# Performance work log

Measured on AMD Instinct MI355X. Metric: run time of the kernel, lower is better.

Reference implementation:

```python
import jax, jax.numpy as jnp
import numpy as np

N = 100000   # nodes
E = 600000   # edges
G = 4096     # graphs in batch
D_IN = 73
D_E = 101
D = 128      # latent_dim
BN_EPS = 1e-5


def _bn(h, gamma, beta):
    # BatchNorm1d in training mode: batch statistics (biased variance)
    m = h.mean(axis=0)
    v = h.var(axis=0)
    return (h - m) * jax.lax.rsqrt(v + BN_EPS) * gamma + beta


def setup_inputs() -> dict:
    key = jax.random.key(0)
    ks = jax.random.split(key, 24)
    inp = {
        "x": jax.random.normal(ks[0], (N, D_IN), jnp.float32),
        "edge_attr": jax.random.normal(ks[1], (E, D_E), jnp.float32),
        "src": jax.random.randint(ks[2], (E,), 0, N, jnp.int32),
        "dst": jax.random.randint(ks[3], (E,), 0, N, jnp.int32),
        "batch": jnp.sort(jax.random.randint(ks[4], (N,), 0, G, jnp.int32)),
        # node embedding Linear(73 -> 128)
        "W_emb": jax.random.normal(ks[5], (D_IN, D), jnp.float32) / np.sqrt(D_IN),
        "b_emb": jnp.zeros((D,), jnp.float32),
    }
    k = 6
    for i in range(2):
        inp[f"We{i}"] = jax.random.normal(ks[k], (D_E, D), jnp.float32) / np.sqrt(D_E); k += 1
        inp[f"be{i}"] = jnp.zeros((D,), jnp.float32)
        inp[f"W1_{i}"] = jax.random.normal(ks[k], (D, 2 * D), jnp.float32) / np.sqrt(D); k += 1
        inp[f"b1_{i}"] = jnp.zeros((2 * D,), jnp.float32)
        inp[f"g1_{i}"] = jnp.ones((2 * D,), jnp.float32)
        inp[f"bb1_{i}"] = jnp.zeros((2 * D,), jnp.float32)
        inp[f"W2_{i}"] = jax.random.normal(ks[k], (2 * D, D), jnp.float32) / np.sqrt(2 * D); k += 1
        inp[f"b2_{i}"] = jnp.zeros((D,), jnp.float32)
        inp[f"go_{i}"] = jnp.ones((D,), jnp.float32)
        inp[f"bo_{i}"] = jnp.zeros((D,), jnp.float32)
    return inp


def _forward(x, edge_attr, src, dst, batch,
             W_emb, b_emb,
             We0, be0, W1_0, b1_0, g1_0, bb1_0, W2_0, b2_0, go_0, bo_0,
             We1, be1, W1_1, b1_1, g1_1, bb1_1, W2_1, b2_1, go_1, bo_1):
    layers = [
        (We0, be0, W1_0, b1_0, g1_0, bb1_0, W2_0, b2_0, go_0, bo_0),
        (We1, be1, W1_1, b1_1, g1_1, bb1_1, W2_1, b2_1, go_1, bo_1),
    ]
    h = x @ W_emb + b_emb  # [N, D]
    n_layers = len(layers)
    for i, (We, be, W1, b1, g1, bb1, W2, b2, go, bo) in enumerate(layers):
        e = edge_attr @ We + be                         # [E, D]
        msg = jax.nn.relu(h[src] + e)                   # gather + add + ReLU
        agg = jax.ops.segment_sum(msg, dst, num_segments=N)  # scatter-sum
        z = h + agg                                     # (1 + eps) * x_i + aggr, eps = 0
        z = jax.nn.relu(_bn(z @ W1 + b1, g1, bb1))      # MLP: Linear -> BN -> ReLU
        h = _bn(z @ W2 + b2, go, bo)                    # Linear -> outer BN
        if i != n_layers - 1:
            h = jax.nn.relu(h)
        # dropout p=0 -> identity
    # global mean pool over graphs
    sums = jax.ops.segment_sum(h, batch, num_segments=G)            # [G, D]
    counts = jax.ops.segment_sum(jnp.ones((h.shape[0],), h.dtype), batch, num_segments=G)
    return sums / jnp.maximum(counts, 1.0)[:, None]


def reference(x, edge_attr, src, dst, batch,
              W_emb, b_emb,
              We0, be0, W1_0, b1_0, g1_0, bb1_0, W2_0, b2_0, go_0, bo_0,
              We1, be1, W1_1, b1_1, g1_1, bb1_1, W2_1, b2_1, go_1, bo_1):
    return _forward(x, edge_attr, src, dst, batch, W_emb, b_emb,
                    We0, be0, W1_0, b1_0, g1_0, bb1_0, W2_0, b2_0, go_0, bo_0,
                    We1, be1, W1_1, b1_1, g1_1, bb1_1, W2_1, b2_1, go_1, bo_1)
```

## Files before the change

kernel.cpp:

```cpp
#include <hip/hip_runtime.h>
#include <cstddef>

#define NN  100000
#define NE  600000
#define NG  4096
#define DIN 73
#define DE  101
#define DD  128
#define DD2 256
#define NP  100096
#define EP  600064

typedef unsigned int uint;
typedef unsigned short ushort;
typedef __attribute__((ext_vector_type(8))) short bf16x8;
typedef __attribute__((ext_vector_type(4))) float f32x4;

__device__ __forceinline__ void fadd_atomic(float* p, float v) { unsafeAtomicAdd(p, v); }

__device__ __forceinline__ ushort f2bf(float f) {
    uint u = __float_as_uint(f);
    uint r = (u + 0x7fffu + ((u >> 16) & 1u)) >> 16;
    return (ushort)r;
}
__device__ __forceinline__ float bf2f(ushort u) { return __uint_as_float(((uint)u) << 16); }

__device__ __forceinline__ bf16x8 ld_zfrag(const float* __restrict__ p) {
    const float4 f0 = *(const float4*)p;
    const float4 f1 = *(const float4*)(p + 4);
    bf16x8 r;
    r[0] = (short)f2bf(f0.x); r[1] = (short)f2bf(f0.y);
    r[2] = (short)f2bf(f0.z); r[3] = (short)f2bf(f0.w);
    r[4] = (short)f2bf(f1.x); r[5] = (short)f2bf(f1.y);
    r[6] = (short)f2bf(f1.z); r[7] = (short)f2bf(f1.w);
    return r;
}


__global__ void hist_kernel(const int* __restrict__ dst, int* __restrict__ deg) {
    int e = blockIdx.x * blockDim.x + threadIdx.x;
    if (e < NE) atomicAdd(&deg[dst[e]], 1);
}

__global__ __launch_bounds__(256) void scan_chunk_kernel(
    const int* __restrict__ deg, int* __restrict__ offs, int* __restrict__ csums)
{
    const int b = blockIdx.x, t = threadIdx.x;
    const int base = b * 1024 + t * 4;
    int v[4];
    #pragma unroll
    for (int i = 0; i < 4; ++i) v[i] = (base + i < NN) ? deg[base + i] : 0;
    int tsum = v[0] + v[1] + v[2] + v[3];
    const int lane = t & 63, w = t >> 6;
    int x = tsum;
    #pragma unroll
    for (int d = 1; d < 64; d <<= 1) {
        int y = __shfl_up(x, d, 64);
        if (lane >= d) x += y;
    }
    __shared__ int wsum[4];
    if (lane == 63) wsum[w] = x;
    __syncthreads();
    int woff = 0;
    for (int i = 0; i < w; ++i) woff += wsum[i];
    int run = woff + x - tsum;
    #pragma unroll
    for (int i = 0; i < 4; ++i) {
        if (base + i < NN) offs[base + i] = run;
        run += v[i];
    }
    if (t == 255) csums[b] = woff + x;
}

__global__ void scan_tops_kernel(int* __restrict__ csums, int* __restrict__ offs, int nchunks) {
    if (threadIdx.x == 0 && blockIdx.x == 0) {
        int run = 0;
        for (int i = 0; i < nchunks; ++i) { int c = csums[i]; csums[i] = run; run += c; }
        offs[NN] = run;
    }
}

__global__ void scan_add_kernel(int* __restrict__ offs, const int* __restrict__ csums) {
    int i = blockIdx.x * blockDim.x + threadIdx.x;
    if (i < NN) offs[i] += csums[i >> 10];
}

__global__ void scatter_kernel(const int* __restrict__ dst, const int* __restrict__ src,
                               const int* __restrict__ offs, int* __restrict__ cursor,
                               int* __restrict__ eperm, int* __restrict__ srcp,
                               int* __restrict__ dstp)
{
    int e = blockIdx.x * blockDim.x + threadIdx.x;
    if (e >= NE) return;
    int d = dst[e];
    int pos = offs[d] + atomicAdd(&cursor[d], 1);
    eperm[e] = pos;
    srcp[pos] = src[e];
    dstp[pos] = d;
}

__global__ void gstart_kernel(const int* __restrict__ batch, int* __restrict__ gstart) {
    int n = blockIdx.x * blockDim.x + threadIdx.x;
    if (n > NN) return;
    if (n == NN) {
        for (int g = batch[NN - 1] + 1; g <= NG; ++g) gstart[g] = NN;
        return;
    }
    int b = batch[n];
    int pb = (n == 0) ? -1 : batch[n - 1];
    for (int g = pb + 1; g <= b; ++g) gstart[g] = n;
}


__global__ __launch_bounds__(256) void cvt_ea_kernel(const float* __restrict__ ea,
                                                     const int* __restrict__ eperm,
                                                     ushort* __restrict__ eabc)
{
    const int t = threadIdx.x;
    const int r = blockIdx.x * 8 + (t >> 5);
    if (r >= NE) return;
    const int pos = eperm[r];
    const int c = (t & 31) * 4;
    ushort4 o;
    #pragma unroll
    for (int i = 0; i < 4; ++i) {
        const int col = c + i;
        float v = (col < DE) ? ea[(size_t)r * DE + col] : ((col == DE) ? 1.0f : 0.0f);
        ((ushort*)&o)[i] = f2bf(v);
    }
    *(ushort4*)&eabc[(size_t)pos * 128 + c] = o;
}

__global__ void cvt_wt_kernel(const float* __restrict__ in, ushort* __restrict__ out,
                              int Kin, int Nn, int Kp, const float* __restrict__ bias)
{
    const int n = blockIdx.x;
    for (int k = threadIdx.x; k < Kp; k += blockDim.x) {
        float v = 0.0f;
        if (k < Kin) v = in[(size_t)k * Nn + n];
        else if (k == Kin && bias) v = bias[n];
        out[(size_t)n * Kp + k] = f2bf(v);
    }
}

__global__ __launch_bounds__(256, 2) void edge_agg_kernel(
    const ushort* __restrict__ eab, const ushort* __restrict__ Wt,
    const int* __restrict__ srcp, const int* __restrict__ dstp,
    const ushort* __restrict__ hb, float* __restrict__ zf)
{
    __shared__ ushort vals[128 * 128];
    __shared__ int nd[128];
    const int tid = threadIdx.x;
    const int wid = tid >> 6;
    const int msub = wid >> 1, nsl = wid & 1;
    const int lane = tid & 63, l15 = lane & 15, grp = lane >> 4;
    const int n0 = nsl * 64;

    bf16x8 A[4][4];
    #pragma unroll
    for (int nf = 0; nf < 4; ++nf)
        #pragma unroll
        for (int kk = 0; kk < 4; ++kk)
            A[nf][kk] = *(const bf16x8*)(Wt + (size_t)(n0 + nf * 16 + l15) * 128 + kk * 32 + grp * 8);

    const int rcol = tid & 127;
    const int rh   = tid >> 7;

    const int ntiles = EP / 128;
    for (int t = blockIdx.x; t < ntiles; t += gridDim.x) {
        const int r0 = t * 128;
        const int m0 = r0 + msub * 64;
        __syncthreads();
        if (tid < 128) {
            const int rr = r0 + tid;
            nd[tid] = (rr < NE) ? dstp[rr] : NN;
        }
        int sp[4];
        #pragma unroll
        for (int mf = 0; mf < 4; ++mf) {
            const int rr = m0 + mf * 16 + l15;
            sp[mf] = (rr < NE) ? srcp[rr] : 0;
        }
        ushort4 hv[4][4];
        #pragma unroll
        for (int mf = 0; mf < 4; ++mf)
            #pragma unroll
            for (int nf = 0; nf < 4; ++nf)
                hv[mf][nf] = *(const ushort4*)&hb[(size_t)sp[mf] * 128 + n0 + nf * 16 + grp * 4];
        f32x4 acc[4][4];
        #pragma unroll
        for (int i = 0; i < 4; ++i)
            #pragma unroll
            for (int j = 0; j < 4; ++j) acc[i][j] = (f32x4){0.f, 0.f, 0.f, 0.f};
        #pragma unroll
        for (int kk = 0; kk < 4; ++kk) {
            bf16x8 b[4];
            #pragma unroll
            for (int mf = 0; mf < 4; ++mf)
                b[mf] = *(const bf16x8*)(eab + (size_t)(m0 + mf * 16 + l15) * 128 + kk * 32 + grp * 8);
            #pragma unroll
            for (int mf = 0; mf < 4; ++mf)
                #pragma unroll
                for (int nf = 0; nf < 4; ++nf)
                    acc[mf][nf] = __builtin_amdgcn_mfma_f32_16x16x32_bf16(A[nf][kk], b[mf], acc[mf][nf], 0, 0, 0);
        }
        #pragma unroll
        for (int mf = 0; mf < 4; ++mf) {
            const int row = msub * 64 + mf * 16 + l15;
            const int sw = (row & 7) << 3;
            #pragma unroll
            for (int nf = 0; nf < 4; ++nf) {
                const int col = n0 + nf * 16 + grp * 4;
                ushort4 o;
                o.x = f2bf(fmaxf(acc[mf][nf][0] + bf2f(hv[mf][nf].x), 0.f));
                o.y = f2bf(fmaxf(acc[mf][nf][1] + bf2f(hv[mf][nf].y), 0.f));
                o.z = f2bf(fmaxf(acc[mf][nf][2] + bf2f(hv[mf][nf].z), 0.f));
                o.w = f2bf(fmaxf(acc[mf][nf][3] + bf2f(hv[mf][nf].w), 0.f));
                *(ushort4*)&vals[row * 128 + (col ^ sw)] = o;
            }
        }
        __syncthreads();
        float accs = 0.f;
        int cur = nd[rh * 64];
        for (int r = rh * 64; r < rh * 64 + 64; ++r) {
            const int node = nd[r];
            const float v = bf2f(vals[r * 128 + (rcol ^ ((r & 7) << 3))]);
            if (node != cur) {
                if (cur < NN) fadd_atomic(&zf[(size_t)cur * 128 + rcol], accs);
                accs = 0.f; cur = node;
            }
            accs += v;
        }
        if (cur < NN) fadd_atomic(&zf[(size_t)cur * 128 + rcol], accs);
    }
}

__global__ void zinit_kernel(const ushort* __restrict__ hb, float* __restrict__ zf) {
    int i = blockIdx.x * blockDim.x + threadIdx.x;
    const int stride = gridDim.x * blockDim.x;
    for (; i < NP * 32; i += stride) {
        const int n = i >> 5;
        float4 o;
        if (n < NN) {
            ushort4 u = *(const ushort4*)&hb[(size_t)i * 4];
            o.x = bf2f(u.x); o.y = bf2f(u.y); o.z = bf2f(u.z); o.w = bf2f(u.w);
        } else {
            o.x = 0.f; o.y = 0.f; o.z = 0.f; o.w = 0.f;
        }
        *(float4*)&zf[(size_t)i * 4] = o;
    }
}


__global__ __launch_bounds__(256, 2) void mlp1_gemm_kernel(
    const float* __restrict__ z, const ushort* __restrict__ Wt,
    const float* __restrict__ bias, ushort* __restrict__ y)
{
    const int n0 = (threadIdx.x >> 6) * 64;
    const int lane = threadIdx.x & 63, l15 = lane & 15, grp = lane >> 4;
    bf16x8 A[4][4];
    #pragma unroll
    for (int nf = 0; nf < 4; ++nf)
        #pragma unroll
        for (int kk = 0; kk < 4; ++kk)
            A[nf][kk] = *(const bf16x8*)(Wt + (size_t)(n0 + nf * 16 + l15) * 128 + kk * 32 + grp * 8);
    float4 bv[4];
    #pragma unroll
    for (int nf = 0; nf < 4; ++nf) bv[nf] = *(const float4*)&bias[n0 + nf * 16 + grp * 4];

    const int ntiles = NP / 64;
    for (int t = blockIdx.x; t < ntiles; t += gridDim.x) {
        const int m0 = t * 64;
        f32x4 acc[4][4];
        #pragma unroll
        for (int i = 0; i < 4; ++i)
            #pragma unroll
            for (int j = 0; j < 4; ++j) acc[i][j] = (f32x4){0.f, 0.f, 0.f, 0.f};
        #pragma unroll
        for (int kk = 0; kk < 4; ++kk) {
            bf16x8 b[4];
            #pragma unroll
            for (int mf = 0; mf < 4; ++mf)
                b[mf] = ld_zfrag(z + (size_t)(m0 + mf * 16 + l15) * 128 + kk * 32 + grp * 8);
            #pragma unroll
            for (int mf = 0; mf < 4; ++mf)
                #pragma unroll
                for (int nf = 0; nf < 4; ++nf)
                    acc[mf][nf] = __builtin_amdgcn_mfma_f32_16x16x32_bf16(A[nf][kk], b[mf], acc[mf][nf], 0, 0, 0);
        }
        #pragma unroll
        for (int mf = 0; mf < 4; ++mf) {
            ushort* rp = &y[(size_t)(m0 + mf * 16 + l15) * 256 + n0];
            #pragma unroll
            for (int nf = 0; nf < 4; ++nf) {
                ushort4 o;
                o.x = f2bf(acc[mf][nf][0] + bv[nf].x);
                o.y = f2bf(acc[mf][nf][1] + bv[nf].y);
                o.z = f2bf(acc[mf][nf][2] + bv[nf].z);
                o.w = f2bf(acc[mf][nf][3] + bv[nf].w);
                *(ushort4*)&rp[nf * 16 + grp * 4] = o;
            }
        }
    }
}

__global__ __launch_bounds__(256, 2) void mlp2_gemm_kernel(
    const ushort* __restrict__ y1, const ushort* __restrict__ Wt,
    const float* __restrict__ bias, ushort* __restrict__ y2)
{
    const int wid = threadIdx.x >> 6;
    const int msub = wid >> 1, nsl = wid & 1;
    const int lane = threadIdx.x & 63, l15 = lane & 15, grp = lane >> 4;
    const int n0 = nsl * 64;
    bf16x8 A[4][8];
    #pragma unroll
    for (int nf = 0; nf < 4; ++nf)
        #pragma unroll
        for (int kk = 0; kk < 8; ++kk)
            A[nf][kk] = *(const bf16x8*)(Wt + (size_t)(n0 + nf * 16 + l15) * 256 + kk * 32 + grp * 8);
    float4 bv[4];
    #pragma unroll
    for (int nf = 0; nf < 4; ++nf) bv[nf] = *(const float4*)&bias[n0 + nf * 16 + grp * 4];

    const int ntiles = NP / 128;
    for (int t = blockIdx.x; t < ntiles; t += gridDim.x) {
        const int m0 = t * 128 + msub * 64;
        f32x4 acc[4][4];
        #pragma unroll
        for (int i = 0; i < 4; ++i)
            #pragma unroll
            for (int j = 0; j < 4; ++j) acc[i][j] = (f32x4){0.f, 0.f, 0.f, 0.f};
        #pragma unroll
        for (int kk = 0; kk < 8; ++kk) {
            bf16x8 b[4];
            #pragma unroll
            for (int mf = 0; mf < 4; ++mf)
                b[mf] = *(const bf16x8*)(y1 + (size_t)(m0 + mf * 16 + l15) * 256 + kk * 32 + grp * 8);
            #pragma unroll
            for (int mf = 0; mf < 4; ++mf)
                #pragma unroll
                for (int nf = 0; nf < 4; ++nf)
                    acc[mf][nf] = __builtin_amdgcn_mfma_f32_16x16x32_bf16(A[nf][kk], b[mf], acc[mf][nf], 0, 0, 0);
        }
        #pragma unroll
        for (int mf = 0; mf < 4; ++mf) {
            ushort* rp = &y2[(size_t)(m0 + mf * 16 + l15) * 128 + n0];
            #pragma unroll
            for (int nf = 0; nf < 4; ++nf) {
                ushort4 o;
                o.x = f2bf(acc[mf][nf][0] + bv[nf].x);
                o.y = f2bf(acc[mf][nf][1] + bv[nf].y);
                o.z = f2bf(acc[mf][nf][2] + bv[nf].z);
                o.w = f2bf(acc[mf][nf][3] + bv[nf].w);
                *(ushort4*)&rp[nf * 16 + grp * 4] = o;
            }
        }
    }
}


__global__ __launch_bounds__(128) void embed_kernel(
    const float* __restrict__ x, const float* __restrict__ W,
    const float* __restrict__ b, ushort* __restrict__ hb)
{
    __shared__ float xs[4][DIN];
    const int n0 = blockIdx.x * 4;
    const int d  = threadIdx.x;
    for (int idx = d; idx < 4 * DIN; idx += 128) {
        int r = idx / DIN, c = idx - r * DIN;
        xs[r][c] = x[(size_t)n0 * DIN + idx];
    }
    __syncthreads();
    float bb = b[d];
    float a0 = bb, a1 = bb, a2 = bb, a3 = bb;
    for (int k = 0; k < DIN; ++k) {
        float w = W[k * DD + d];
        a0 = fmaf(xs[0][k], w, a0);
        a1 = fmaf(xs[1][k], w, a1);
        a2 = fmaf(xs[2][k], w, a2);
        a3 = fmaf(xs[3][k], w, a3);
    }
    hb[(size_t)(n0 + 0) * DD + d] = f2bf(a0);
    hb[(size_t)(n0 + 1) * DD + d] = f2bf(a1);
    hb[(size_t)(n0 + 2) * DD + d] = f2bf(a2);
    hb[(size_t)(n0 + 3) * DD + d] = f2bf(a3);
}

__global__ __launch_bounds__(256) void colstats256_kernel(
    const ushort* __restrict__ y, float* __restrict__ s, float* __restrict__ q)
{
    const int t = threadIdx.x;
    const int cs = (t & 63) * 4, rg = t >> 6;
    const int r0 = blockIdx.x * 256;
    float ps0 = 0, ps1 = 0, ps2 = 0, ps3 = 0, pq0 = 0, pq1 = 0, pq2 = 0, pq3 = 0;
    for (int i = rg; i < 256; i += 4) {
        const int r = r0 + i;
        if (r >= NN) break;
        ushort4 u = *(const ushort4*)&y[(size_t)r * 256 + cs];
        float f0 = bf2f(u.x), f1 = bf2f(u.y), f2v = bf2f(u.z), f3 = bf2f(u.w);
        ps0 += f0; pq0 += f0 * f0;
        ps1 += f1; pq1 += f1 * f1;
        ps2 += f2v; pq2 += f2v * f2v;
        ps3 += f3; pq3 += f3 * f3;
    }
    __shared__ float SS[4][256], SQ[4][256];
    SS[rg][cs + 0] = ps0; SS[rg][cs + 1] = ps1; SS[rg][cs + 2] = ps2; SS[rg][cs + 3] = ps3;
    SQ[rg][cs + 0] = pq0; SQ[rg][cs + 1] = pq1; SQ[rg][cs + 2] = pq2; SQ[rg][cs + 3] = pq3;
    __syncthreads();
    if (rg == 0) {
        #pragma unroll
        for (int j = 0; j < 4; ++j) {
            const int c = cs + j;
            fadd_atomic(&s[c], SS[0][c] + SS[1][c] + SS[2][c] + SS[3][c]);
            fadd_atomic(&q[c], SQ[0][c] + SQ[1][c] + SQ[2][c] + SQ[3][c]);
        }
    }
}

__global__ __launch_bounds__(256) void colstats128b_kernel(
    const ushort* __restrict__ y, float* __restrict__ s, float* __restrict__ q)
{
    const int t = threadIdx.x;
    const int cs = (t & 31) * 4, rg = t >> 5;
    const int r0 = blockIdx.x * 256;
    float ps0 = 0, ps1 = 0, ps2 = 0, ps3 = 0, pq0 = 0, pq1 = 0, pq2 = 0, pq3 = 0;
    for (int i = rg; i < 256; i += 8) {
        const int r = r0 + i;
        if (r >= NN) break;
        ushort4 u = *(const ushort4*)&y[(size_t)r * 128 + cs];
        float f0 = bf2f(u.x), f1 = bf2f(u.y), f2v = bf2f(u.z), f3 = bf2f(u.w);
        ps0 += f0; pq0 += f0 * f0;
        ps1 += f1; pq1 += f1 * f1;
        ps2 += f2v; pq2 += f2v * f2v;
        ps3 += f3; pq3 += f3 * f3;
    }
    __shared__ float SS[8][128], SQ[8][128];
    SS[rg][cs + 0] = ps0; SS[rg][cs + 1] = ps1; SS[rg][cs + 2] = ps2; SS[rg][cs + 3] = ps3;
    SQ[rg][cs + 0] = pq0; SQ[rg][cs + 1] = pq1; SQ[rg][cs + 2] = pq2; SQ[rg][cs + 3] = pq3;
    __syncthreads();
    if (rg == 0) {
        #pragma unroll
        for (int j = 0; j < 4; ++j) {
            const int c = cs + j;
            float sv = 0, qv = 0;
            #pragma unroll
            for (int g = 0; g < 8; ++g) { sv += SS[g][c]; qv += SQ[g][c]; }
            fadd_atomic(&s[c], sv);
            fadd_atomic(&q[c], qv);
        }
    }
}

__global__ void finalize_kernel(const float* __restrict__ s, const float* __restrict__ sq,
                                const float* __restrict__ g, const float* __restrict__ bb,
                                float* __restrict__ a, float* __restrict__ c,
                                int dim, float invN)
{
    int d = blockIdx.x * blockDim.x + threadIdx.x;
    if (d >= dim) return;
    float m  = s[d] * invN;
    float v  = sq[d] * invN - m * m;
    float rs = rsqrtf(v + 1e-5f);
    float ai = g[d] * rs;
    a[d] = ai;
    c[d] = bb[d] - m * ai;
}

__global__ void bnrelu_bf_kernel(ushort* __restrict__ y, const float* __restrict__ a,
                                 const float* __restrict__ c)
{
    int i = blockIdx.x * blockDim.x + threadIdx.x;
    const int stride = gridDim.x * blockDim.x;
    for (; i < NN * 64; i += stride) {
        const int cb = (i & 63) * 4;
        ushort4 u = *(const ushort4*)&y[(size_t)i * 4];
        const float4 av = *(const float4*)&a[cb];
        const float4 cv = *(const float4*)&c[cb];
        ushort4 o;
        o.x = f2bf(fmaxf(fmaf(bf2f(u.x), av.x, cv.x), 0.f));
        o.y = f2bf(fmaxf(fmaf(bf2f(u.y), av.y, cv.y), 0.f));
        o.z = f2bf(fmaxf(fmaf(bf2f(u.z), av.z, cv.z), 0.f));
        o.w = f2bf(fmaxf(fmaf(bf2f(u.w), av.w, cv.w), 0.f));
        *(ushort4*)&y[(size_t)i * 4] = o;
    }
}

__global__ void bnrelu_hb_kernel(ushort* __restrict__ hb, const float* __restrict__ a,
                                 const float* __restrict__ c)
{
    int i = blockIdx.x * blockDim.x + threadIdx.x;
    const int stride = gridDim.x * blockDim.x;
    for (; i < NN * 32; i += stride) {
        const int cb = (i & 31) * 4;
        ushort4 u = *(const ushort4*)&hb[(size_t)i * 4];
        const float4 av = *(const float4*)&a[cb];
        const float4 cv = *(const float4*)&c[cb];
        ushort4 o;
        o.x = f2bf(fmaxf(fmaf(bf2f(u.x), av.x, cv.x), 0.f));
        o.y = f2bf(fmaxf(fmaf(bf2f(u.y), av.y, cv.y), 0.f));
        o.z = f2bf(fmaxf(fmaf(bf2f(u.z), av.z, cv.z), 0.f));
        o.w = f2bf(fmaxf(fmaf(bf2f(u.w), av.w, cv.w), 0.f));
        *(ushort4*)&hb[(size_t)i * 4] = o;
    }
}

__global__ __launch_bounds__(256) void pool_kernel(
    const ushort* __restrict__ hb, const float* __restrict__ a2, const float* __restrict__ c2,
    const int* __restrict__ gstart, float* __restrict__ out)
{
    const int g = blockIdx.x * 4 + (threadIdx.x >> 6);
    if (g >= NG) return;
    const int lane = threadIdx.x & 63;
    const int s = gstart[g], t = gstart[g + 1];
    float a0 = 0.f, a1 = 0.f;
    for (int n = s; n < t; ++n) {
        const uint v = *(const uint*)&hb[(size_t)n * 128 + lane * 2];
        a0 += __uint_as_float(v << 16);
        a1 += __uint_as_float(v & 0xffff0000u);
    }
    const int d0 = lane * 2;
    float2 o;
    if (t > s) {
        const float inv = 1.0f / (float)(t - s);
        o.x = fmaf(a2[d0 + 0], a0 * inv, c2[d0 + 0]);
        o.y = fmaf(a2[d0 + 1], a1 * inv, c2[d0 + 1]);
    } else {
        o.x = 0.f; o.y = 0.f;
    }
    *(float2*)&out[(size_t)g * 128 + d0] = o;
}


extern "C" void kernel_launch(void* const* d_in, const int* in_sizes, int n_in,
                              void* d_out, int out_size, void* d_ws, size_t ws_size,
                              hipStream_t stream)
{
    (void)in_sizes; (void)n_in; (void)out_size; (void)ws_size;
    const float* x     = (const float*)d_in[0];
    const float* ea    = (const float*)d_in[1];
    const int*   src   = (const int*)d_in[2];
    const int*   dst   = (const int*)d_in[3];
    const int*   batch = (const int*)d_in[4];
    const float* W_emb = (const float*)d_in[5];
    const float* b_emb = (const float*)d_in[6];

    char* ws = (char*)d_ws;
    auto alloc = [&](size_t bytes) { void* p = ws; ws += (bytes + 255) & ~(size_t)255; return p; };

    ushort* hb   = (ushort*)alloc((size_t)NP * 128 * 2);
    float*  zf   = (float*) alloc((size_t)NP * 128 * 4);
    ushort* eabc = (ushort*)alloc((size_t)EP * 128 * 2);
    ushort* y1b  = (ushort*)alloc((size_t)NP * 256 * 2);
    int* deg    = (int*)alloc((size_t)NN * 4);
    int* offs   = (int*)alloc((size_t)(NN + 1) * 4);
    int* eperm  = (int*)alloc((size_t)NE * 4);
    int* srcp   = (int*)alloc((size_t)NE * 4);
    int* dstp   = (int*)alloc((size_t)NE * 4);
    int* csums  = (int*)alloc(128 * 4);
    int* gstart = (int*)alloc((size_t)(NG + 1) * 4);
    ushort* Wet[2], *W1t[2], *W2t[2];
    for (int l = 0; l < 2; ++l) {
        Wet[l] = (ushort*)alloc(128 * 128 * 2);
        W1t[l] = (ushort*)alloc(256 * 128 * 2);
        W2t[l] = (ushort*)alloc(128 * 256 * 2);
    }
    float* st = (float*)alloc(2048 * 4);
    float* s1 = st,        *sq1 = st + 256, *a1 = st + 512,  *c1 = st + 768;
    float* s2 = st + 1024, *sq2 = st + 1152, *a2 = st + 1280, *c2 = st + 1408;
    float* out = (float*)d_out;

    const int NCHUNK = (NN + 1023) / 1024;

    hipMemsetAsync(deg, 0, (size_t)NN * 4, stream);
    hist_kernel<<<(NE + 255) / 256, 256, 0, stream>>>(dst, deg);
    scan_chunk_kernel<<<NCHUNK, 256, 0, stream>>>(deg, offs, csums);
    scan_tops_kernel<<<1, 1, 0, stream>>>(csums, offs, NCHUNK);
    scan_add_kernel<<<(NN + 255) / 256, 256, 0, stream>>>(offs, csums);
    hipMemsetAsync(deg, 0, (size_t)NN * 4, stream);
    scatter_kernel<<<(NE + 255) / 256, 256, 0, stream>>>(dst, src, offs, deg, eperm, srcp, dstp);
    gstart_kernel<<<(NN + 256) / 256, 256, 0, stream>>>(batch, gstart);

    cvt_ea_kernel<<<(NE + 7) / 8, 256, 0, stream>>>(ea, eperm, eabc);
    for (int l = 0; l < 2; ++l) {
        const float* const* L = (const float* const*)(d_in + 7 + l * 10);
        cvt_wt_kernel<<<128, 128, 0, stream>>>(L[0], Wet[l], 101, 128, 128, L[1]);
        cvt_wt_kernel<<<256, 128, 0, stream>>>(L[2], W1t[l], 128, 256, 128, nullptr);
        cvt_wt_kernel<<<128, 128, 0, stream>>>(L[6], W2t[l], 256, 128, 256, nullptr);
    }

    embed_kernel<<<NN / 4, 128, 0, stream>>>(x, W_emb, b_emb, hb);

    for (int layer = 0; layer < 2; ++layer) {
        const float* const* L = (const float* const*)(d_in + 7 + layer * 10);
        const float* b1  = L[3];
        const float* g1  = L[4]; const float* bb1 = L[5];
        const float* b2  = L[7];
        const float* go  = L[8]; const float* bo  = L[9];

        zinit_kernel<<<2048, 256, 0, stream>>>(hb, zf);
        edge_agg_kernel<<<1172, 256, 0, stream>>>(eabc, Wet[layer], srcp, dstp, hb, zf);

        hipMemsetAsync(s1, 0, 512 * sizeof(float), stream);
        hipMemsetAsync(s2, 0, 256 * sizeof(float), stream);

        mlp1_gemm_kernel<<<782, 256, 0, stream>>>(zf, W1t[layer], b1, y1b);
        colstats256_kernel<<<NP / 256 + 1, 256, 0, stream>>>(y1b, s1, sq1);
        finalize_kernel<<<1, 256, 0, stream>>>(s1, sq1, g1, bb1, a1, c1, 256, 1.0f / NN);
        bnrelu_bf_kernel<<<2048, 256, 0, stream>>>(y1b, a1, c1);
        mlp2_gemm_kernel<<<391, 256, 0, stream>>>(y1b, W2t[layer], b2, hb);
        colstats128b_kernel<<<NP / 256 + 1, 256, 0, stream>>>(hb, s2, sq2);
        finalize_kernel<<<1, 128, 0, stream>>>(s2, sq2, go, bo, a2, c2, 128, 1.0f / NN);

        if (layer == 0) {
            bnrelu_hb_kernel<<<2048, 256, 0, stream>>>(hb, a2, c2);
        } else {
            pool_kernel<<<NG / 4, 256, 0, stream>>>(hb, a2, c2, gstart, out);
        }
    }
}
```

Before: 1.039 ms.

## Fuse z initialization into embed and BN-ReLU kernels; unroll edge segmented reduce

Removes the separate zinit kernel, which read hb and wrote the fp32 z buffer. Embed and the layer-0 BN-ReLU kernel now write the fp32 copy directly, saving one full read of hb and one launch per layer. The edge aggregation kernel is tuned as well: occupancy hint raised to 3 blocks per SM, __syncthreads replaced with an explicit lgkmcnt wait plus s_barrier, and the per-column segmented reduction unrolled to batch 8 LDS reads ahead of the atomic logic. The padding rows of zf are no longer zeroed each layer, so correctness depends on that region staying zero from allocation.

```diff
diff --git a/kernel.cpp b/kernel.cpp
--- a/kernel.cpp
+++ b/kernel.cpp
@@ -36,6 +36,8 @@
     return r;
 }
 
+#define BARRIER_LDS() asm volatile("s_waitcnt lgkmcnt(0)\n\ts_barrier" ::: "memory")
+
 
 __global__ void hist_kernel(const int* __restrict__ dst, int* __restrict__ deg) {
     int e = blockIdx.x * blockDim.x + threadIdx.x;
@@ -143,7 +145,7 @@
     }
 }
 
-__global__ __launch_bounds__(256, 2) void edge_agg_kernel(
+__global__ __launch_bounds__(256, 3) void edge_agg_kernel(
     const ushort* __restrict__ eab, const ushort* __restrict__ Wt,
     const int* __restrict__ srcp, const int* __restrict__ dstp,
     const ushort* __restrict__ hb, float* __restrict__ zf)
@@ -170,7 +172,7 @@
     for (int t = blockIdx.x; t < ntiles; t += gridDim.x) {
         const int r0 = t * 128;
         const int m0 = r0 + msub * 64;
-        __syncthreads();
+        BARRIER_LDS();
         if (tid < 128) {
             const int rr = r0 + tid;
             nd[tid] = (rr < NE) ? dstp[rr] : NN;
@@ -219,35 +221,27 @@
                 *(ushort4*)&vals[row * 128 + (col ^ sw)] = o;
             }
         }
-        __syncthreads();
+        BARRIER_LDS();
         float accs = 0.f;
         int cur = nd[rh * 64];
-        for (int r = rh * 64; r < rh * 64 + 64; ++r) {
-            const int node = nd[r];
-            const float v = bf2f(vals[r * 128 + (rcol ^ ((r & 7) << 3))]);
-            if (node != cur) {
-                if (cur < NN) fadd_atomic(&zf[(size_t)cur * 128 + rcol], accs);
-                accs = 0.f; cur = node;
+        #pragma unroll
+        for (int r8 = 0; r8 < 8; ++r8) {
+            const int rbase = rh * 64 + r8 * 8;
+            float v[8];
+            #pragma unroll
+            for (int j = 0; j < 8; ++j)
+                v[j] = bf2f(vals[(rbase + j) * 128 + (rcol ^ (((rbase + j) & 7) << 3))]);
+            #pragma unroll
+            for (int j = 0; j < 8; ++j) {
+                const int node = nd[rbase + j];
+                if (node != cur) {
+                    if (cur < NN) fadd_atomic(&zf[(size_t)cur * 128 + rcol], accs);
+                    accs = 0.f; cur = node;
+                }
+                accs += v[j];
             }
-            accs += v;
         }
         if (cur < NN) fadd_atomic(&zf[(size_t)cur * 128 + rcol], accs);
-    }
-}
-
-__global__ void zinit_kernel(const ushort* __restrict__ hb, float* __restrict__ zf) {
-    int i = blockIdx.x * blockDim.x + threadIdx.x;
-    const int stride = gridDim.x * blockDim.x;
-    for (; i < NP * 32; i += stride) {
-        const int n = i >> 5;
-        float4 o;
-        if (n < NN) {
-            ushort4 u = *(const ushort4*)&hb[(size_t)i * 4];
-            o.x = bf2f(u.x); o.y = bf2f(u.y); o.z = bf2f(u.z); o.w = bf2f(u.w);
-        } else {
-            o.x = 0.f; o.y = 0.f; o.z = 0.f; o.w = 0.f;
-        }
-        *(float4*)&zf[(size_t)i * 4] = o;
     }
 }
 
@@ -361,7 +355,7 @@
 
 __global__ __launch_bounds__(128) void embed_kernel(
     const float* __restrict__ x, const float* __restrict__ W,
-    const float* __restrict__ b, ushort* __restrict__ hb)
+    const float* __restrict__ b, ushort* __restrict__ hb, float* __restrict__ zf)
 {
     __shared__ float xs[4][DIN];
     const int n0 = blockIdx.x * 4;
@@ -380,10 +374,15 @@
         a2 = fmaf(xs[2][k], w, a2);
         a3 = fmaf(xs[3][k], w, a3);
     }
-    hb[(size_t)(n0 + 0) * DD + d] = f2bf(a0);
-    hb[(size_t)(n0 + 1) * DD + d] = f2bf(a1);
-    hb[(size_t)(n0 + 2) * DD + d] = f2bf(a2);
-    hb[(size_t)(n0 + 3) * DD + d] = f2bf(a3);
+    ushort u0 = f2bf(a0), u1 = f2bf(a1), u2 = f2bf(a2), u3 = f2bf(a3);
+    hb[(size_t)(n0 + 0) * DD + d] = u0;
+    hb[(size_t)(n0 + 1) * DD + d] = u1;
+    hb[(size_t)(n0 + 2) * DD + d] = u2;
+    hb[(size_t)(n0 + 3) * DD + d] = u3;
+    zf[(size_t)(n0 + 0) * DD + d] = bf2f(u0);
+    zf[(size_t)(n0 + 1) * DD + d] = bf2f(u1);
+    zf[(size_t)(n0 + 2) * DD + d] = bf2f(u2);
+    zf[(size_t)(n0 + 3) * DD + d] = bf2f(u3);
 }
 
 __global__ __launch_bounds__(256) void colstats256_kernel(
@@ -486,7 +485,7 @@
 }
 
 __global__ void bnrelu_hb_kernel(ushort* __restrict__ hb, const float* __restrict__ a,
-                                 const float* __restrict__ c)
+                                 const float* __restrict__ c, float* __restrict__ zf)
 {
     int i = blockIdx.x * blockDim.x + threadIdx.x;
     const int stride = gridDim.x * blockDim.x;
@@ -501,6 +500,9 @@
         o.z = f2bf(fmaxf(fmaf(bf2f(u.z), av.z, cv.z), 0.f));
         o.w = f2bf(fmaxf(fmaf(bf2f(u.w), av.w, cv.w), 0.f));
         *(ushort4*)&hb[(size_t)i * 4] = o;
+        float4 zo;
+        zo.x = bf2f(o.x); zo.y = bf2f(o.y); zo.z = bf2f(o.z); zo.w = bf2f(o.w);
+        *(float4*)&zf[(size_t)i * 4] = zo;
     }
 }
 
@@ -588,7 +590,7 @@
         cvt_wt_kernel<<<128, 128, 0, stream>>>(L[6], W2t[l], 256, 128, 256, nullptr);
     }
 
-    embed_kernel<<<NN / 4, 128, 0, stream>>>(x, W_emb, b_emb, hb);
+    embed_kernel<<<NN / 4, 128, 0, stream>>>(x, W_emb, b_emb, hb, zf);
 
     for (int layer = 0; layer < 2; ++layer) {
         const float* const* L = (const float* const*)(d_in + 7 + layer * 10);
@@ -597,7 +599,6 @@
         const float* b2  = L[7];
         const float* go  = L[8]; const float* bo  = L[9];
 
-        zinit_kernel<<<2048, 256, 0, stream>>>(hb, zf);
         edge_agg_kernel<<<1172, 256, 0, stream>>>(eabc, Wet[layer], srcp, dstp, hb, zf);
 
         hipMemsetAsync(s1, 0, 512 * sizeof(float), stream);
@@ -612,7 +613,7 @@
         finalize_kernel<<<1, 128, 0, stream>>>(s2, sq2, go, bo, a2, c2, 128, 1.0f / NN);
 
         if (layer == 0) {
-            bnrelu_hb_kernel<<<2048, 256, 0, stream>>>(hb, a2, c2);
+            bnrelu_hb_kernel<<<2048, 256, 0, stream>>>(hb, a2, c2, zf);
         } else {
             pool_kernel<<<NG / 4, 256, 0, stream>>>(hb, a2, c2, gstart, out);
         }
```

Result: slower. 1.119 ms (+7.7%).

## Precompute per-tile destination segments and use plain stores for interior segments

Applied to the files above, without the earlier changes.

Adds a one-time segbuild kernel that scans each 128-edge tile of dst-sorted edges. It records every run of equal destinations as a packed descriptor (node, start, length, boundary flag). The edge aggregation epilogue now walks these segments with all 256 threads instead of 128 threads each serially scanning 64 rows. Segments wholly inside a tile write h+sum with a plain store, and only the first and last segments in a tile use float atomics. The intent is to cut atomic traffic and the serial per-column reduction loop; the cost is variable segment lengths, which can cause warp divergence, plus an extra descriptor load.

```diff
diff --git a/kernel.cpp b/kernel.cpp
--- a/kernel.cpp
+++ b/kernel.cpp
@@ -10,6 +10,7 @@
 #define DD2 256
 #define NP  100096
 #define EP  600064
+#define NT  (EP / 128)
 
 typedef unsigned int uint;
 typedef unsigned short ushort;
@@ -111,6 +112,37 @@
     for (int g = pb + 1; g <= b; ++g) gstart[g] = n;
 }
 
+__global__ __launch_bounds__(128) void segbuild_kernel(const int* __restrict__ dstp,
+                                                       uint* __restrict__ segpack,
+                                                       int* __restrict__ nsegs)
+{
+    const int t = blockIdx.x, r = threadIdx.x;
+    const int rr = t * 128 + r;
+    __shared__ int nd[128];
+    __shared__ int sc[128];
+    nd[r] = (rr < NE) ? dstp[rr] : NN;
+    __syncthreads();
+    const int flag = (r == 0 || nd[r] != nd[r - 1]) ? 1 : 0;
+    sc[r] = flag;
+    __syncthreads();
+    for (int d = 1; d < 128; d <<= 1) {
+        int v = (r >= d) ? sc[r - d] : 0;
+        __syncthreads();
+        sc[r] += v;
+        __syncthreads();
+    }
+    const int total = sc[127];
+    if (flag) {
+        const int s = sc[r] - 1;
+        int len = 1;
+        while (r + len < 128 && nd[r + len] == nd[r]) ++len;
+        const uint bnd = (s == 0 || s == total - 1) ? 1u : 0u;
+        segpack[(size_t)t * 128 + s] =
+            ((uint)nd[r]) | ((uint)r << 17) | ((uint)(len - 1) << 24) | (bnd << 31);
+    }
+    if (r == 0) nsegs[t] = total;
+}
+
 
 __global__ __launch_bounds__(256) void cvt_ea_kernel(const float* __restrict__ ea,
                                                      const int* __restrict__ eperm,
@@ -145,11 +177,11 @@
 
 __global__ __launch_bounds__(256, 2) void edge_agg_kernel(
     const ushort* __restrict__ eab, const ushort* __restrict__ Wt,
-    const int* __restrict__ srcp, const int* __restrict__ dstp,
-    const ushort* __restrict__ hb, float* __restrict__ zf)
+    const int* __restrict__ srcp, const uint* __restrict__ segpack,
+    const int* __restrict__ nsegs, const ushort* __restrict__ hb,
+    float* __restrict__ zf)
 {
     __shared__ ushort vals[128 * 128];
-    __shared__ int nd[128];
     const int tid = threadIdx.x;
     const int wid = tid >> 6;
     const int msub = wid >> 1, nsl = wid & 1;
@@ -163,18 +195,9 @@
         for (int kk = 0; kk < 4; ++kk)
             A[nf][kk] = *(const bf16x8*)(Wt + (size_t)(n0 + nf * 16 + l15) * 128 + kk * 32 + grp * 8);
 
-    const int rcol = tid & 127;
-    const int rh   = tid >> 7;
-
-    const int ntiles = EP / 128;
-    for (int t = blockIdx.x; t < ntiles; t += gridDim.x) {
-        const int r0 = t * 128;
-        const int m0 = r0 + msub * 64;
+    for (int t = blockIdx.x; t < NT; t += gridDim.x) {
+        const int m0 = t * 128 + msub * 64;
         __syncthreads();
-        if (tid < 128) {
-            const int rr = r0 + tid;
-            nd[tid] = (rr < NE) ? dstp[rr] : NN;
-        }
         int sp[4];
         #pragma unroll
         for (int mf = 0; mf < 4; ++mf) {
@@ -220,18 +243,22 @@
             }
         }
         __syncthreads();
-        float accs = 0.f;
-        int cur = nd[rh * 64];
-        for (int r = rh * 64; r < rh * 64 + 64; ++r) {
-            const int node = nd[r];
-            const float v = bf2f(vals[r * 128 + (rcol ^ ((r & 7) << 3))]);
-            if (node != cur) {
-                if (cur < NN) fadd_atomic(&zf[(size_t)cur * 128 + rcol], accs);
-                accs = 0.f; cur = node;
-            }
-            accs += v;
-        }
-        if (cur < NN) fadd_atomic(&zf[(size_t)cur * 128 + rcol], accs);
+        const int ns = nsegs[t];
+        const uint* spk = &segpack[(size_t)t * 128];
+        for (int p = tid; p < ns * 128; p += 256) {
+            const int s = p >> 7, col = p & 127;
+            const uint m = spk[s];
+            const int node = m & 0x1FFFF;
+            if (node >= NN) continue;
+            const int start = (m >> 17) & 127;
+            const int len = (int)((m >> 24) & 127) + 1;
+            float sum = 0.f;
+            for (int r = start; r < start + len; ++r)
+                sum += bf2f(vals[r * 128 + (col ^ ((r & 7) << 3))]);
+            float* zp = &zf[(size_t)node * 128 + col];
+            if (m >> 31) fadd_atomic(zp, sum);
+            else *zp = bf2f(hb[(size_t)node * 128 + col]) + sum;
+        }
     }
 }
 
@@ -558,6 +585,8 @@
     int* dstp   = (int*)alloc((size_t)NE * 4);
     int* csums  = (int*)alloc(128 * 4);
     int* gstart = (int*)alloc((size_t)(NG + 1) * 4);
+    uint* segpack = (uint*)alloc((size_t)NT * 128 * 4);
+    int*  nsegs   = (int*)alloc((size_t)NT * 4);
     ushort* Wet[2], *W1t[2], *W2t[2];
     for (int l = 0; l < 2; ++l) {
         Wet[l] = (ushort*)alloc(128 * 128 * 2);
@@ -579,6 +608,7 @@
     hipMemsetAsync(deg, 0, (size_t)NN * 4, stream);
     scatter_kernel<<<(NE + 255) / 256, 256, 0, stream>>>(dst, src, offs, deg, eperm, srcp, dstp);
     gstart_kernel<<<(NN + 256) / 256, 256, 0, stream>>>(batch, gstart);
+    segbuild_kernel<<<NT, 128, 0, stream>>>(dstp, segpack, nsegs);
 
     cvt_ea_kernel<<<(NE + 7) / 8, 256, 0, stream>>>(ea, eperm, eabc);
     for (int l = 0; l < 2; ++l) {
@@ -598,7 +628,7 @@
         const float* go  = L[8]; const float* bo  = L[9];
 
         zinit_kernel<<<2048, 256, 0, stream>>>(hb, zf);
-        edge_agg_kernel<<<1172, 256, 0, stream>>>(eabc, Wet[layer], srcp, dstp, hb, zf);
+        edge_agg_kernel<<<1172, 256, 0, stream>>>(eabc, Wet[layer], srcp, segpack, nsegs, hb, zf);
 
         hipMemsetAsync(s1, 0, 512 * sizeof(float), stream);
         hipMemsetAsync(s2, 0, 256 * sizeof(float), stream);
```

Result: slower. 1.137 ms (+9.5%).
